# Performance work log

Hardware: AMD Instinct MI355X
Metric: run time of the kernel (lower is better)

## Reference

```python
import jax, jax.numpy as jnp
import numpy as np

T, D, H, E, V = 256, 512, 256, 256, 8192  # steps, max_ast_depth, hidden=units, emb dim, vocab


def setup_inputs() -> dict:
    key = jax.random.key(0)
    ks = jax.random.split(key, 12)
    s = 1.0 / np.sqrt(H)
    u = lambda k, shp: jax.random.uniform(k, shp, jnp.float32, -s, s)
    return {
        "nodes": jax.random.randint(ks[0], (T, D), 0, V),
        "edges": jax.random.randint(ks[1], (T, D), 0, 2).astype(bool),
        "initial_state": jax.random.normal(ks[2], (1, D, H), jnp.float32),
        "emb": jax.random.normal(ks[3], (V, E), jnp.float32) * 0.02,
        "c_Wih": u(ks[4], (3 * H, E)), "c_Whh": u(ks[5], (3 * H, H)),
        "c_bih": u(ks[6], (3 * H,)), "c_bhh": u(ks[7], (3 * H,)),
        "s_Wih": u(ks[8], (3 * H, E)), "s_Whh": u(ks[9], (3 * H, H)),
        "s_bih": u(ks[10], (3 * H,)), "s_bhh": u(ks[11], (3 * H,)),
    }


def _gru_cell(x, h, Wih, Whh, bih, bhh):
    # torch GRU cell math: gates ordered (r, z, n)
    gi = x @ Wih.T + bih           # [D, 3H]
    gh = h @ Whh.T + bhh           # [D, 3H]
    ir, iz, in_ = jnp.split(gi, 3, axis=-1)
    hr, hz, hn = jnp.split(gh, 3, axis=-1)
    r = jax.nn.sigmoid(ir + hr)
    z = jax.nn.sigmoid(iz + hz)
    n = jnp.tanh(in_ + r * hn)
    return (1.0 - z) * n + z * h   # [D, H]


def reference(nodes, edges, initial_state, emb,
              c_Wih, c_Whh, c_bih, c_bhh,
              s_Wih, s_Whh, s_bih, s_bhh):
    # Single-layer dual GRU: per step, run both GRUs on the same state and
    # route per node via the boolean edge mask (child vs sibling).
    def step(h, te):
        node_t, edge_t = te            # [D] int, [D] bool
        x = emb[node_t]                # [D, E] embedding gather
        hc = _gru_cell(x, h, c_Wih, c_Whh, c_bih, c_bhh)
        hs = _gru_cell(x, h, s_Wih, s_Whh, s_bih, s_bhh)
        h_new = jnp.where(edge_t[:, None], hc, hs)  # [D, H]
        return h_new, h_new            # output == new state for 1-layer GRU (seq_len 1)

    h_final, outs = jax.lax.scan(step, initial_state[0], (nodes, edges))
    # match torch shapes: outputs [T, D, 1, H], state [num_layers, D, H]
    return outs[:, :, None, :], h_final[None]
```

## Files before the change

kernel.cpp:

```cpp
#include <hip/hip_runtime.h>
#include <stdint.h>


#define TT   256
#define DDIM 512
#define LSTR 264

typedef float    float4v __attribute__((ext_vector_type(4)));
typedef short    short8  __attribute__((ext_vector_type(8)));
typedef uint32_t uint4v  __attribute__((ext_vector_type(4)));

__device__ __forceinline__ unsigned short f2bf(float f){
  uint32_t u = __float_as_uint(f);
  u += 0x7fffu + ((u >> 16) & 1u);
  return (unsigned short)(u >> 16);
}
__device__ __forceinline__ float bf2f(unsigned short h){
  return __uint_as_float(((uint32_t)h) << 16);
}

__global__ __launch_bounds__(256, 1)
void treernn_main(const int* __restrict__ nodes,
                  const unsigned char* __restrict__ edges,
                  const unsigned char* __restrict__ hinit,
                  const unsigned char* __restrict__ emb,
                  const unsigned char* __restrict__ cWih, const unsigned char* __restrict__ cWhh,
                  const unsigned char* __restrict__ cbih, const unsigned char* __restrict__ cbhh,
                  const unsigned char* __restrict__ sWih, const unsigned char* __restrict__ sWhh,
                  const unsigned char* __restrict__ sbih, const unsigned char* __restrict__ sbhh,
                  unsigned char* __restrict__ out,
                  unsigned char* __restrict__ ws)
{
  __shared__ __align__(16) unsigned short xs[2][32 * LSTR];
  __shared__ __align__(16) unsigned short hstg[32 * LSTR];
  __shared__ float hnewstg[32 * 17];
  __shared__ int det[8];

  const int tid   = threadIdx.x;
  const int lane  = tid & 63;
  const int wv    = tid >> 6;
  const int gru   = wv >> 1;
  const int mtile = wv & 1;
  const int quad  = lane >> 4;
  const int l16   = lane & 15;

  const int g     = blockIdx.x >> 4;
  const int slice = blockIdx.x & 15;
  const int col   = slice * 16 + l16;
  const int d0    = g * 32;
  const int rowb  = mtile * 16 + quad * 4;

  if (tid < 8) det[tid] = 0;
  __syncthreads();
  {
    const unsigned short* hu = (const unsigned short*)hinit;
    int ce = 0;
    for (int i = tid; i < 4096; i += 256){
      const int e = (hu[i] >> 7) & 0xFF;
      ce += (e >= 100 && e <= 130) ? 1 : 0;
    }
    atomicAdd(&det[0], ce);
    const uint32_t* ewp = (const uint32_t*)edges;
    int b01 = 0, w01 = 0, wf = 0, hb = 0;
    for (int i = tid; i < 512; i += 256){
      const uint32_t w = ewp[i];
      w01 += (w <= 1u) ? 1 : 0;
      wf  += (w == 0u || w == 0x3F800000u) ? 1 : 0;
      const uint32_t h0 = w & 0xFFFFu, h1 = w >> 16;
      hb  += ((h0 == 0u || h0 == 0x3F80u) ? 1 : 0) + ((h1 == 0u || h1 == 0x3F80u) ? 1 : 0);
      b01 += (((w      ) & 0xFFu) <= 1u ? 1 : 0) + (((w >> 8 ) & 0xFFu) <= 1u ? 1 : 0)
           + (((w >> 16) & 0xFFu) <= 1u ? 1 : 0) + (((w >> 24)        ) <= 1u ? 1 : 0);
    }
    atomicAdd(&det[1], b01); atomicAdd(&det[2], w01);
    atomicAdd(&det[3], wf);  atomicAdd(&det[4], hb);
  }
  __syncthreads();
  const int fdt = (det[0] >= 3480) ? 1 : 0;
  int efmt;
  if      (det[2] == 512)  efmt = 1;
  else if (det[1] == 2048) efmt = 0;
  else if (det[4] == 1024) efmt = 3;
  else if (det[3] == 512)  efmt = 2;
  else                     efmt = 0;

  uint32_t*       flg = (uint32_t*)ws;
  unsigned short* xb  = (unsigned short*)(ws + 8192);

  const unsigned char* Wihp = gru ? sWih : cWih;
  const unsigned char* Whhp = gru ? sWhh : cWhh;
  const unsigned char* bihp = gru ? sbih : cbih;
  const unsigned char* bhhp = gru ? sbhh : cbhh;

  float bI[3], bH[3];
  #pragma unroll
  for (int ga = 0; ga < 3; ++ga){
    if (fdt){
      bI[ga] = bf2f(((const unsigned short*)bihp)[ga * 256 + col]);
      bH[ga] = bf2f(((const unsigned short*)bhhp)[ga * 256 + col]);
    } else {
      bI[ga] = ((const float*)bihp)[ga * 256 + col];
      bH[ga] = ((const float*)bhhp)[ga * 256 + col];
    }
  }

  short8 wI[3][8], wH[3][8];
  for (int ga = 0; ga < 3; ++ga){
    const int rw = ga * 256 + col;
    for (int kc = 0; kc < 8; ++kc){
      const int ke = kc * 32 + quad * 8;
      if (fdt){
        wI[ga][kc] = *(const short8*)((const unsigned short*)Wihp + (size_t)rw * 256 + ke);
        wH[ga][kc] = *(const short8*)((const unsigned short*)Whhp + (size_t)rw * 256 + ke);
      } else {
        const float* pI = (const float*)Wihp + (size_t)rw * 256 + ke;
        const float* pH = (const float*)Whhp + (size_t)rw * 256 + ke;
        short8 va, vb;
        #pragma unroll
        for (int j = 0; j < 8; ++j){ va[j] = (short)f2bf(pI[j]); vb[j] = (short)f2bf(pH[j]); }
        wI[ga][kc] = va; wH[ga][kc] = vb;
      }
    }
  }

  {
    const int r = tid >> 3, c8 = (tid & 7) * 32;
    const int node = nodes[d0 + r];
    unsigned short* xdst = &xs[0][r * LSTR + c8];
    unsigned short* hdst = &hstg[r * LSTR + c8];
    if (fdt){
      const uint4v* sx = (const uint4v*)((const unsigned short*)emb   + (size_t)node * 256 + c8);
      const uint4v* sh = (const uint4v*)((const unsigned short*)hinit + (size_t)(d0 + r) * 256 + c8);
      #pragma unroll
      for (int j = 0; j < 4; ++j){ ((uint4v*)xdst)[j] = sx[j]; ((uint4v*)hdst)[j] = sh[j]; }
    } else {
      const float* sx = (const float*)emb   + (size_t)node * 256 + c8;
      const float* sh = (const float*)hinit + (size_t)(d0 + r) * 256 + c8;
      #pragma unroll
      for (int q = 0; q < 4; ++q){
        short8 vx, vh;
        #pragma unroll
        for (int j = 0; j < 8; ++j){ vx[j] = (short)f2bf(sx[q*8+j]); vh[j] = (short)f2bf(sh[q*8+j]); }
        *(short8*)&xdst[q * 8] = vx;
        *(short8*)&hdst[q * 8] = vh;
      }
    }
  }

  int ef[4];
  {
    const int base = d0 + rowb;
    if (efmt == 0){      for (int r = 0; r < 4; ++r) ef[r] = edges[base + r] != 0; }
    else if (efmt == 1){ for (int r = 0; r < 4; ++r) ef[r] = ((const int*)edges)[base + r] != 0; }
    else if (efmt == 3){ for (int r = 0; r < 4; ++r) ef[r] = ((const unsigned short*)edges)[base + r] != 0; }
    else {               for (int r = 0; r < 4; ++r) ef[r] = ((const float*)edges)[base + r] != 0.0f; }
  }
  __syncthreads();

  uint64_t gv[8];
  const int grow = tid >> 3;
  const int gchk = tid & 7;

  for (int t = 0; t < TT; ++t){
    if (slice == 0 && t >= 2){
      if (fdt){
        uint64_t* od = (uint64_t*)((unsigned short*)out + (size_t)(t - 2) * 131072
                                   + (size_t)(d0 + grow) * 256) + gchk;
        #pragma unroll
        for (int k = 0; k < 8; ++k) od[k * 8] = gv[k];
      } else {
        float* ob = (float*)out + (size_t)(t - 2) * 131072 + (size_t)(d0 + grow) * 256 + gchk * 4;
        #pragma unroll
        for (int k = 0; k < 8; ++k){
          float4v f;
          #pragma unroll
          for (int j = 0; j < 4; ++j) f[j] = bf2f((unsigned short)(gv[k] >> (16 * j)));
          *(float4v*)(ob + k * 32) = f;
        }
      }
    }

    float4v aI[3], aH[3];
    #pragma unroll
    for (int ga = 0; ga < 3; ++ga) aI[ga] = (float4v){bI[ga], bI[ga], bI[ga], bI[ga]};
    {
      const unsigned short* xc = xs[t & 1];
      #pragma unroll
      for (int kc = 0; kc < 8; ++kc){
        short8 a = *(const short8*)&xc[(mtile * 16 + l16) * LSTR + kc * 32 + quad * 8];
        #pragma unroll
        for (int ga = 0; ga < 3; ++ga)
          aI[ga] = __builtin_amdgcn_mfma_f32_16x16x32_bf16(a, wI[ga][kc], aI[ga], 0, 0, 0);
      }
    }

    float hold[4];
    if (t == 0){
      #pragma unroll
      for (int r = 0; r < 4; ++r){
        const size_t idx = (size_t)(d0 + rowb + r) * 256 + col;
        hold[r] = fdt ? bf2f(((const unsigned short*)hinit)[idx]) : ((const float*)hinit)[idx];
      }
    } else {
      #pragma unroll
      for (int r = 0; r < 4; ++r) hold[r] = hnewstg[(rowb + r) * 17 + l16];
    }

    if (t > 0){
      const uint32_t target = (uint32_t)t;
      const uint32_t* fp = flg + g * 64 + lane;
      uint32_t fv = __hip_atomic_load(fp, __ATOMIC_RELAXED, __HIP_MEMORY_SCOPE_AGENT);
      int guard = 0;
      while (__ballot(fv < target) != 0ull){
        __builtin_amdgcn_s_sleep(1);
        fv = __hip_atomic_load(fp, __ATOMIC_RELAXED, __HIP_MEMORY_SCOPE_AGENT);
        if (++guard > (1 << 17)) break;
      }
      __atomic_signal_fence(__ATOMIC_SEQ_CST);
      const uint64_t* src = (const uint64_t*)(xb + (size_t)(t & 1) * 131072
                                                 + (size_t)(d0 + grow) * 256) + gchk;
      #pragma unroll
      for (int k = 0; k < 8; ++k)
        gv[k] = __hip_atomic_load(src + k * 8, __ATOMIC_RELAXED, __HIP_MEMORY_SCOPE_AGENT);
      unsigned short* dst = &hstg[grow * LSTR + gchk * 4];
      #pragma unroll
      for (int k = 0; k < 8; ++k) *(uint64_t*)&dst[k * 32] = gv[k];
    }
    __syncthreads();

    #pragma unroll
    for (int ga = 0; ga < 3; ++ga) aH[ga] = (float4v){bH[ga], bH[ga], bH[ga], bH[ga]};
    #pragma unroll
    for (int kc = 0; kc < 8; ++kc){
      short8 a = *(const short8*)&hstg[(mtile * 16 + l16) * LSTR + kc * 32 + quad * 8];
      #pragma unroll
      for (int ga = 0; ga < 3; ++ga)
        aH[ga] = __builtin_amdgcn_mfma_f32_16x16x32_bf16(a, wH[ga][kc], aH[ga], 0, 0, 0);
    }

    float hnv[4]; int mine[4];
    #pragma unroll
    for (int r = 0; r < 4; ++r){
      const float pr = aI[0][r] + aH[0][r];
      const float pz = aI[1][r] + aH[1][r];
      const float R  = 1.0f / (1.0f + exp2f(-1.4426950408889634f * pr));
      const float Z  = 1.0f / (1.0f + exp2f(-1.4426950408889634f * pz));
      float ag = aI[2][r] + R * aH[2][r];
      ag = fminf(30.0f, fmaxf(-30.0f, ag));
      const float ex = exp2f(-2.8853900817779268f * ag);
      const float N  = (1.0f - ex) / (1.0f + ex);
      hnv[r]  = N + Z * (hold[r] - N);
      mine[r] = ((ef[r] != 0) == (gru == 0)) ? 1 : 0;
    }

    #pragma unroll
    for (int r = 0; r < 4; ++r){
      if (mine[r]) hnewstg[(rowb + r) * 17 + l16] = hnv[r];
      const uint32_t bb = (uint32_t)f2bf(hnv[r]);
      const uint32_t ob = (uint32_t)__shfl_xor((int)bb, 1, 64);
      if (mine[r] && !(lane & 1)){
        unsigned short* p = xb + (size_t)((t + 1) & 1) * 131072
                               + (size_t)(d0 + rowb + r) * 256 + col;
        __hip_atomic_store((uint32_t*)p, bb | (ob << 16),
                           __ATOMIC_RELAXED, __HIP_MEMORY_SCOPE_AGENT);
      }
    }

    __atomic_signal_fence(__ATOMIC_SEQ_CST);
    __builtin_amdgcn_s_waitcnt(0x0F70);
    __atomic_signal_fence(__ATOMIC_SEQ_CST);
    if (lane == 0)
      __hip_atomic_store(flg + g * 64 + slice * 4 + wv, (uint32_t)(t + 1),
                         __ATOMIC_RELAXED, __HIP_MEMORY_SCOPE_AGENT);

    if (t < TT - 1){
      const int r = tid >> 3, c8 = (tid & 7) * 32;
      const int node = nodes[(t + 1) * DDIM + d0 + r];
      unsigned short* dst = &xs[(t + 1) & 1][r * LSTR + c8];
      if (fdt){
        const uint4v* s = (const uint4v*)((const unsigned short*)emb + (size_t)node * 256 + c8);
        uint4v rv[4];
        #pragma unroll
        for (int j = 0; j < 4; ++j) rv[j] = s[j];
        #pragma unroll
        for (int j = 0; j < 4; ++j) ((uint4v*)dst)[j] = rv[j];
      } else {
        const float* s = (const float*)emb + (size_t)node * 256 + c8;
        float4v rv[8];
        #pragma unroll
        for (int j = 0; j < 8; ++j) rv[j] = ((const float4v*)s)[j];
        #pragma unroll
        for (int q = 0; q < 4; ++q){
          short8 v;
          #pragma unroll
          for (int j = 0; j < 8; ++j){ const int e2 = q*8+j; v[j] = (short)f2bf(rv[e2>>2][e2&3]); }
          *(short8*)&dst[q * 8] = v;
        }
      }
      const int base = (t + 1) * DDIM + d0 + rowb;
      if (efmt == 0){      for (int r2 = 0; r2 < 4; ++r2) ef[r2] = edges[base + r2] != 0; }
      else if (efmt == 1){ for (int r2 = 0; r2 < 4; ++r2) ef[r2] = ((const int*)edges)[base + r2] != 0; }
      else if (efmt == 3){ for (int r2 = 0; r2 < 4; ++r2) ef[r2] = ((const unsigned short*)edges)[base + r2] != 0; }
      else {               for (int r2 = 0; r2 < 4; ++r2) ef[r2] = ((const float*)edges)[base + r2] != 0.0f; }
    }

    __syncthreads();
  }

  if (slice == 0){
    if (fdt){
      uint64_t* od = (uint64_t*)((unsigned short*)out + (size_t)254 * 131072
                                 + (size_t)(d0 + grow) * 256) + gchk;
      #pragma unroll
      for (int k = 0; k < 8; ++k) od[k * 8] = gv[k];
    } else {
      float* ob = (float*)out + (size_t)254 * 131072 + (size_t)(d0 + grow) * 256 + gchk * 4;
      #pragma unroll
      for (int k = 0; k < 8; ++k){
        float4v f;
        #pragma unroll
        for (int j = 0; j < 4; ++j) f[j] = bf2f((unsigned short)(gv[k] >> (16 * j)));
        *(float4v*)(ob + k * 32) = f;
      }
    }

    const uint32_t* fp = flg + g * 64 + lane;
    uint32_t fv = __hip_atomic_load(fp, __ATOMIC_RELAXED, __HIP_MEMORY_SCOPE_AGENT);
    int guard = 0;
    while (__ballot(fv < 256u) != 0ull){
      __builtin_amdgcn_s_sleep(1);
      fv = __hip_atomic_load(fp, __ATOMIC_RELAXED, __HIP_MEMORY_SCOPE_AGENT);
      if (++guard > (1 << 17)) break;
    }
    __atomic_signal_fence(__ATOMIC_SEQ_CST);
    const uint64_t* src = (const uint64_t*)(xb +  (size_t)(d0 + grow) * 256) + gchk;
    uint64_t ev[8];
    #pragma unroll
    for (int k = 0; k < 8; ++k)
      ev[k] = __hip_atomic_load(src + k * 8, __ATOMIC_RELAXED, __HIP_MEMORY_SCOPE_AGENT);
    if (fdt){
      unsigned short* o16 = (unsigned short*)out;
      uint64_t* o1 = (uint64_t*)(o16 + (size_t)255 * 131072 + (size_t)(d0 + grow) * 256) + gchk;
      uint64_t* o2 = (uint64_t*)(o16 + (size_t)256 * 131072 + (size_t)(d0 + grow) * 256) + gchk;
      #pragma unroll
      for (int k = 0; k < 8; ++k){ o1[k * 8] = ev[k]; o2[k * 8] = ev[k]; }
    } else {
      float* o1 = (float*)out + (size_t)255 * 131072 + (size_t)(d0 + grow) * 256 + gchk * 4;
      float* o2 = (float*)out + (size_t)256 * 131072 + (size_t)(d0 + grow) * 256 + gchk * 4;
      #pragma unroll
      for (int k = 0; k < 8; ++k){
        float4v f;
        #pragma unroll
        for (int j = 0; j < 4; ++j) f[j] = bf2f((unsigned short)(ev[k] >> (16 * j)));
        *(float4v*)(o1 + k * 32) = f;
        *(float4v*)(o2 + k * 32) = f;
      }
    }
  }
}

extern "C" void kernel_launch(void* const* d_in, const int* in_sizes, int n_in,
                              void* d_out, int out_size, void* d_ws, size_t ws_size,
                              hipStream_t stream)
{
  const int*           nodes = (const int*)d_in[0];
  const unsigned char* edges = (const unsigned char*)d_in[1];
  const unsigned char* hinit = (const unsigned char*)d_in[2];
  const unsigned char* emb   = (const unsigned char*)d_in[3];
  const unsigned char* cWih  = (const unsigned char*)d_in[4];
  const unsigned char* cWhh  = (const unsigned char*)d_in[5];
  const unsigned char* cbih  = (const unsigned char*)d_in[6];
  const unsigned char* cbhh  = (const unsigned char*)d_in[7];
  const unsigned char* sWih  = (const unsigned char*)d_in[8];
  const unsigned char* sWhh  = (const unsigned char*)d_in[9];
  const unsigned char* sbih  = (const unsigned char*)d_in[10];
  const unsigned char* sbhh  = (const unsigned char*)d_in[11];
  (void)in_sizes; (void)n_in; (void)out_size; (void)ws_size;

  hipMemsetAsync(d_ws, 0, 8192, stream);

  treernn_main<<<dim3(256), dim3(256), 0, stream>>>(
      nodes, edges, hinit, emb, cWih, cWhh, cbih, cbhh, sWih, sWhh, sbih, sbhh,
      (unsigned char*)d_out, (unsigned char*)d_ws);
}
```

Before: 1.337 ms.

## Repartition GRU work into 16-row groups with 8 column slices per group

Each block now handles 16 rows and 32 output columns (8 slices per row group) instead of 32 rows and 16 columns. Every block writes its own output columns straight from registers rather than having slice 0 re-read the exchanged hidden state for the whole group. The previous hidden state is kept in shared memory, which drops the global read of hinit at t=0 inside the loop. The intent is to shrink per-block staging and the critical path of the per-step cross-block exchange, and to spread output stores across all blocks. In exchange the flag layout changes and output writes become narrower scattered 32-bit stores.

```diff
diff --git a/kernel.cpp b/kernel.cpp
--- a/kernel.cpp
+++ b/kernel.cpp
@@ -18,6 +18,7 @@
 __device__ __forceinline__ float bf2f(unsigned short h){
   return __uint_as_float(((uint32_t)h) << 16);
 }
+__device__ __forceinline__ float4v splat4(float v){ return (float4v){v, v, v, v}; }
 
 __global__ __launch_bounds__(256, 1)
 void treernn_main(const int* __restrict__ nodes,
@@ -31,24 +32,25 @@
                   unsigned char* __restrict__ out,
                   unsigned char* __restrict__ ws)
 {
-  __shared__ __align__(16) unsigned short xs[2][32 * LSTR];
-  __shared__ __align__(16) unsigned short hstg[32 * LSTR];
-  __shared__ float hnewstg[32 * 17];
+  __shared__ __align__(16) unsigned short xs[2][16 * LSTR];
+  __shared__ __align__(16) unsigned short hstg[16 * LSTR];
+  __shared__ float hold[16 * 33];
   __shared__ int det[8];
 
-  const int tid   = threadIdx.x;
-  const int lane  = tid & 63;
-  const int wv    = tid >> 6;
-  const int gru   = wv >> 1;
-  const int mtile = wv & 1;
-  const int quad  = lane >> 4;
-  const int l16   = lane & 15;
-
-  const int g     = blockIdx.x >> 4;
-  const int slice = blockIdx.x & 15;
-  const int col   = slice * 16 + l16;
-  const int d0    = g * 32;
-  const int rowb  = mtile * 16 + quad * 4;
+  const int tid  = threadIdx.x;
+  const int lane = tid & 63;
+  const int wv   = tid >> 6;
+  const int gru  = wv >> 1;
+  const int ch   = wv & 1;
+  const int quad = lane >> 4;
+  const int l16  = lane & 15;
+  const int bid  = blockIdx.x;
+
+  const int G    = bid >> 3;
+  const int cs   = bid & 7;
+  const int d0   = G * 16;
+  const int colw = ch * 16 + l16;
+  const int col  = cs * 32 + colw;
 
   if (tid < 8) det[tid] = 0;
   __syncthreads();
@@ -84,7 +86,7 @@
   else                     efmt = 0;
 
   uint32_t*       flg = (uint32_t*)ws;
-  unsigned short* xb  = (unsigned short*)(ws + 8192);
+  unsigned short* xbp = (unsigned short*)(ws + 16384);
 
   const unsigned char* Wihp = gru ? sWih : cWih;
   const unsigned char* Whhp = gru ? sWhh : cWhh;
@@ -123,32 +125,41 @@
   }
 
   {
-    const int r = tid >> 3, c8 = (tid & 7) * 32;
-    const int node = nodes[d0 + r];
-    unsigned short* xdst = &xs[0][r * LSTR + c8];
-    unsigned short* hdst = &hstg[r * LSTR + c8];
+    const int row = tid >> 4, cb = (tid & 15) * 16;
+    const int nd = nodes[d0 + row];
+    unsigned short* xdst = &xs[0][row * LSTR + cb];
+    unsigned short* hdst = &hstg[row * LSTR + cb];
     if (fdt){
-      const uint4v* sx = (const uint4v*)((const unsigned short*)emb   + (size_t)node * 256 + c8);
-      const uint4v* sh = (const uint4v*)((const unsigned short*)hinit + (size_t)(d0 + r) * 256 + c8);
-      #pragma unroll
-      for (int j = 0; j < 4; ++j){ ((uint4v*)xdst)[j] = sx[j]; ((uint4v*)hdst)[j] = sh[j]; }
+      const unsigned short* sx = (const unsigned short*)emb   + (size_t)nd * 256 + cb;
+      const unsigned short* sh = (const unsigned short*)hinit + (size_t)(d0 + row) * 256 + cb;
+      *(uint4v*)xdst       = *(const uint4v*)sx;
+      *(uint4v*)(xdst + 8) = *(const uint4v*)(sx + 8);
+      *(uint4v*)hdst       = *(const uint4v*)sh;
+      *(uint4v*)(hdst + 8) = *(const uint4v*)(sh + 8);
     } else {
-      const float* sx = (const float*)emb   + (size_t)node * 256 + c8;
-      const float* sh = (const float*)hinit + (size_t)(d0 + r) * 256 + c8;
-      #pragma unroll
-      for (int q = 0; q < 4; ++q){
-        short8 vx, vh;
-        #pragma unroll
-        for (int j = 0; j < 8; ++j){ vx[j] = (short)f2bf(sx[q*8+j]); vh[j] = (short)f2bf(sh[q*8+j]); }
-        *(short8*)&xdst[q * 8] = vx;
-        *(short8*)&hdst[q * 8] = vh;
-      }
-    }
-  }
-
+      const float* sx = (const float*)emb   + (size_t)nd * 256 + cb;
+      const float* sh = (const float*)hinit + (size_t)(d0 + row) * 256 + cb;
+      short8 v0, v1, w0, w1;
+      #pragma unroll
+      for (int j = 0; j < 8; ++j){
+        v0[j] = (short)f2bf(sx[j]); v1[j] = (short)f2bf(sx[8 + j]);
+        w0[j] = (short)f2bf(sh[j]); w1[j] = (short)f2bf(sh[8 + j]);
+      }
+      *(short8*)xdst = v0; *(short8*)(xdst + 8) = v1;
+      *(short8*)hdst = w0; *(short8*)(hdst + 8) = w1;
+    }
+    if (gru == 0){
+      #pragma unroll
+      for (int r = 0; r < 4; ++r){
+        const size_t si = (size_t)(d0 + quad * 4 + r) * 256 + col;
+        hold[(quad * 4 + r) * 33 + colw] =
+            fdt ? bf2f(((const unsigned short*)hinit)[si]) : ((const float*)hinit)[si];
+      }
+    }
+  }
   int ef[4];
   {
-    const int base = d0 + rowb;
+    const int base = d0 + quad * 4;
     if (efmt == 0){      for (int r = 0; r < 4; ++r) ef[r] = edges[base + r] != 0; }
     else if (efmt == 1){ for (int r = 0; r < 4; ++r) ef[r] = ((const int*)edges)[base + r] != 0; }
     else if (efmt == 3){ for (int r = 0; r < 4; ++r) ef[r] = ((const unsigned short*)edges)[base + r] != 0; }
@@ -156,58 +167,54 @@
   }
   __syncthreads();
 
-  uint64_t gv[8];
-  const int grow = tid >> 3;
-  const int gchk = tid & 7;
+  const int grow = tid >> 4;
+  const int gsub = tid & 15;
+  uint32_t* flgG = flg + G * 32;
+
+  uint32_t sPk[4] = {0, 0, 0, 0};
+  float    sCd[4] = {0, 0, 0, 0};
+  int      sMn[4] = {0, 0, 0, 0};
 
   for (int t = 0; t < TT; ++t){
-    if (slice == 0 && t >= 2){
-      if (fdt){
-        uint64_t* od = (uint64_t*)((unsigned short*)out + (size_t)(t - 2) * 131072
-                                   + (size_t)(d0 + grow) * 256) + gchk;
-        #pragma unroll
-        for (int k = 0; k < 8; ++k) od[k * 8] = gv[k];
-      } else {
-        float* ob = (float*)out + (size_t)(t - 2) * 131072 + (size_t)(d0 + grow) * 256 + gchk * 4;
-        #pragma unroll
-        for (int k = 0; k < 8; ++k){
-          float4v f;
-          #pragma unroll
-          for (int j = 0; j < 4; ++j) f[j] = bf2f((unsigned short)(gv[k] >> (16 * j)));
-          *(float4v*)(ob + k * 32) = f;
+    if (t > 0){
+      #pragma unroll
+      for (int r = 0; r < 4; ++r){
+        const int row = quad * 4 + r;
+        if (fdt){
+          if (sMn[r] && !(lane & 1)){
+            unsigned short* o16 = (unsigned short*)out;
+            *(uint32_t*)(o16 + (size_t)(t - 1) * 131072 + (size_t)(d0 + row) * 256 + col) = sPk[r];
+          }
+        } else {
+          if (sMn[r]){
+            float* o32 = (float*)out;
+            o32[(size_t)(t - 1) * 131072 + (size_t)(d0 + row) * 256 + col] = sCd[r];
+          }
         }
       }
     }
 
-    float4v aI[3], aH[3];
-    #pragma unroll
-    for (int ga = 0; ga < 3; ++ga) aI[ga] = (float4v){bI[ga], bI[ga], bI[ga], bI[ga]};
+    float4v aI[3];
+    #pragma unroll
+    for (int ga = 0; ga < 3; ++ga) aI[ga] = splat4(bI[ga]);
     {
       const unsigned short* xc = xs[t & 1];
       #pragma unroll
       for (int kc = 0; kc < 8; ++kc){
-        short8 a = *(const short8*)&xc[(mtile * 16 + l16) * LSTR + kc * 32 + quad * 8];
+        short8 a = *(const short8*)&xc[l16 * LSTR + kc * 32 + quad * 8];
         #pragma unroll
         for (int ga = 0; ga < 3; ++ga)
           aI[ga] = __builtin_amdgcn_mfma_f32_16x16x32_bf16(a, wI[ga][kc], aI[ga], 0, 0, 0);
       }
     }
 
-    float hold[4];
-    if (t == 0){
-      #pragma unroll
-      for (int r = 0; r < 4; ++r){
-        const size_t idx = (size_t)(d0 + rowb + r) * 256 + col;
-        hold[r] = fdt ? bf2f(((const unsigned short*)hinit)[idx]) : ((const float*)hinit)[idx];
-      }
-    } else {
-      #pragma unroll
-      for (int r = 0; r < 4; ++r) hold[r] = hnewstg[(rowb + r) * 17 + l16];
-    }
+    float hold4[4];
+    #pragma unroll
+    for (int r = 0; r < 4; ++r) hold4[r] = hold[(quad * 4 + r) * 33 + colw];
 
     if (t > 0){
       const uint32_t target = (uint32_t)t;
-      const uint32_t* fp = flg + g * 64 + lane;
+      const uint32_t* fp = flgG + (lane & 31);
       uint32_t fv = __hip_atomic_load(fp, __ATOMIC_RELAXED, __HIP_MEMORY_SCOPE_AGENT);
       int guard = 0;
       while (__ballot(fv < target) != 0ull){
@@ -216,28 +223,32 @@
         if (++guard > (1 << 17)) break;
       }
       __atomic_signal_fence(__ATOMIC_SEQ_CST);
-      const uint64_t* src = (const uint64_t*)(xb + (size_t)(t & 1) * 131072
-                                                 + (size_t)(d0 + grow) * 256) + gchk;
-      #pragma unroll
-      for (int k = 0; k < 8; ++k)
-        gv[k] = __hip_atomic_load(src + k * 8, __ATOMIC_RELAXED, __HIP_MEMORY_SCOPE_AGENT);
-      unsigned short* dst = &hstg[grow * LSTR + gchk * 4];
-      #pragma unroll
-      for (int k = 0; k < 8; ++k) *(uint64_t*)&dst[k * 32] = gv[k];
+      const uint64_t* src = (const uint64_t*)(xbp + ((size_t)(t & 1) * 512 + d0 + grow) * 256
+                                                  + gsub * 16);
+      uint64_t a0 = __hip_atomic_load(src + 0, __ATOMIC_RELAXED, __HIP_MEMORY_SCOPE_AGENT);
+      uint64_t a1 = __hip_atomic_load(src + 1, __ATOMIC_RELAXED, __HIP_MEMORY_SCOPE_AGENT);
+      uint64_t a2 = __hip_atomic_load(src + 2, __ATOMIC_RELAXED, __HIP_MEMORY_SCOPE_AGENT);
+      uint64_t a3 = __hip_atomic_load(src + 3, __ATOMIC_RELAXED, __HIP_MEMORY_SCOPE_AGENT);
+      unsigned short* dst = &hstg[grow * LSTR + gsub * 16];
+      *(uint64_t*)(dst + 0)  = a0;
+      *(uint64_t*)(dst + 4)  = a1;
+      *(uint64_t*)(dst + 8)  = a2;
+      *(uint64_t*)(dst + 12) = a3;
     }
     __syncthreads();
 
-    #pragma unroll
-    for (int ga = 0; ga < 3; ++ga) aH[ga] = (float4v){bH[ga], bH[ga], bH[ga], bH[ga]};
+    float4v aH[3];
+    #pragma unroll
+    for (int ga = 0; ga < 3; ++ga) aH[ga] = splat4(bH[ga]);
     #pragma unroll
     for (int kc = 0; kc < 8; ++kc){
-      short8 a = *(const short8*)&hstg[(mtile * 16 + l16) * LSTR + kc * 32 + quad * 8];
+      short8 a = *(const short8*)&hstg[l16 * LSTR + kc * 32 + quad * 8];
       #pragma unroll
       for (int ga = 0; ga < 3; ++ga)
         aH[ga] = __builtin_amdgcn_mfma_f32_16x16x32_bf16(a, wH[ga][kc], aH[ga], 0, 0, 0);
     }
 
-    float hnv[4]; int mine[4];
+    float cand[4]; int mine[4];
     #pragma unroll
     for (int r = 0; r < 4; ++r){
       const float pr = aI[0][r] + aH[0][r];
@@ -248,111 +259,76 @@
       ag = fminf(30.0f, fmaxf(-30.0f, ag));
       const float ex = exp2f(-2.8853900817779268f * ag);
       const float N  = (1.0f - ex) / (1.0f + ex);
-      hnv[r]  = N + Z * (hold[r] - N);
+      cand[r] = N + Z * (hold4[r] - N);
       mine[r] = ((ef[r] != 0) == (gru == 0)) ? 1 : 0;
     }
 
+    const int buf = (t + 1) & 1;
     #pragma unroll
     for (int r = 0; r < 4; ++r){
-      if (mine[r]) hnewstg[(rowb + r) * 17 + l16] = hnv[r];
-      const uint32_t bb = (uint32_t)f2bf(hnv[r]);
+      const int row = quad * 4 + r;
+      if (mine[r]) hold[row * 33 + colw] = cand[r];
+      const uint32_t bb = (uint32_t)f2bf(cand[r]);
       const uint32_t ob = (uint32_t)__shfl_xor((int)bb, 1, 64);
-      if (mine[r] && !(lane & 1)){
-        unsigned short* p = xb + (size_t)((t + 1) & 1) * 131072
-                               + (size_t)(d0 + rowb + r) * 256 + col;
-        __hip_atomic_store((uint32_t*)p, bb | (ob << 16),
+      const uint32_t pk = bb | (ob << 16);
+      sPk[r] = pk; sCd[r] = cand[r]; sMn[r] = mine[r];
+      if (t < TT - 1 && mine[r] && !(lane & 1)){
+        uint32_t* xp = (uint32_t*)&xbp[((size_t)buf * 512 + d0 + row) * 256 + col];
+        __hip_atomic_store(xp, pk, __ATOMIC_RELAXED, __HIP_MEMORY_SCOPE_AGENT);
+      }
+    }
+
+    if (t < TT - 1){
+      __atomic_signal_fence(__ATOMIC_SEQ_CST);
+      __builtin_amdgcn_s_waitcnt(0x0F70);
+      __atomic_signal_fence(__ATOMIC_SEQ_CST);
+      if (lane == 0)
+        __hip_atomic_store(flgG + cs * 4 + wv, (uint32_t)(t + 1),
                            __ATOMIC_RELAXED, __HIP_MEMORY_SCOPE_AGENT);
-      }
-    }
-
-    __atomic_signal_fence(__ATOMIC_SEQ_CST);
-    __builtin_amdgcn_s_waitcnt(0x0F70);
-    __atomic_signal_fence(__ATOMIC_SEQ_CST);
-    if (lane == 0)
-      __hip_atomic_store(flg + g * 64 + slice * 4 + wv, (uint32_t)(t + 1),
-                         __ATOMIC_RELAXED, __HIP_MEMORY_SCOPE_AGENT);
-
-    if (t < TT - 1){
-      const int r = tid >> 3, c8 = (tid & 7) * 32;
-      const int node = nodes[(t + 1) * DDIM + d0 + r];
-      unsigned short* dst = &xs[(t + 1) & 1][r * LSTR + c8];
-      if (fdt){
-        const uint4v* s = (const uint4v*)((const unsigned short*)emb + (size_t)node * 256 + c8);
-        uint4v rv[4];
-        #pragma unroll
-        for (int j = 0; j < 4; ++j) rv[j] = s[j];
-        #pragma unroll
-        for (int j = 0; j < 4; ++j) ((uint4v*)dst)[j] = rv[j];
-      } else {
-        const float* s = (const float*)emb + (size_t)node * 256 + c8;
-        float4v rv[8];
-        #pragma unroll
-        for (int j = 0; j < 8; ++j) rv[j] = ((const float4v*)s)[j];
-        #pragma unroll
-        for (int q = 0; q < 4; ++q){
-          short8 v;
+
+      {
+        const int row = tid >> 4, cb = (tid & 15) * 16;
+        const int nd = nodes[(t + 1) * DDIM + d0 + row];
+        unsigned short* dst = &xs[buf][row * LSTR + cb];
+        if (fdt){
+          const unsigned short* s = (const unsigned short*)emb + (size_t)nd * 256 + cb;
+          uint4v r0 = *(const uint4v*)s;
+          uint4v r1 = *(const uint4v*)(s + 8);
+          *(uint4v*)dst       = r0;
+          *(uint4v*)(dst + 8) = r1;
+        } else {
+          const float* s = (const float*)emb + (size_t)nd * 256 + cb;
+          short8 v0, v1;
           #pragma unroll
-          for (int j = 0; j < 8; ++j){ const int e2 = q*8+j; v[j] = (short)f2bf(rv[e2>>2][e2&3]); }
-          *(short8*)&dst[q * 8] = v;
+          for (int j = 0; j < 8; ++j){ v0[j] = (short)f2bf(s[j]); v1[j] = (short)f2bf(s[8 + j]); }
+          *(short8*)dst       = v0;
+          *(short8*)(dst + 8) = v1;
         }
-      }
-      const int base = (t + 1) * DDIM + d0 + rowb;
-      if (efmt == 0){      for (int r2 = 0; r2 < 4; ++r2) ef[r2] = edges[base + r2] != 0; }
-      else if (efmt == 1){ for (int r2 = 0; r2 < 4; ++r2) ef[r2] = ((const int*)edges)[base + r2] != 0; }
-      else if (efmt == 3){ for (int r2 = 0; r2 < 4; ++r2) ef[r2] = ((const unsigned short*)edges)[base + r2] != 0; }
-      else {               for (int r2 = 0; r2 < 4; ++r2) ef[r2] = ((const float*)edges)[base + r2] != 0.0f; }
+        const int eb = (t + 1) * DDIM + d0 + quad * 4;
+        if (efmt == 0){      for (int r2 = 0; r2 < 4; ++r2) ef[r2] = edges[eb + r2] != 0; }
+        else if (efmt == 1){ for (int r2 = 0; r2 < 4; ++r2) ef[r2] = ((const int*)edges)[eb + r2] != 0; }
+        else if (efmt == 3){ for (int r2 = 0; r2 < 4; ++r2) ef[r2] = ((const unsigned short*)edges)[eb + r2] != 0; }
+        else {               for (int r2 = 0; r2 < 4; ++r2) ef[r2] = ((const float*)edges)[eb + r2] != 0.0f; }
+      }
     }
 
     __syncthreads();
   }
 
-  if (slice == 0){
+  #pragma unroll
+  for (int r = 0; r < 4; ++r){
+    const int row = quad * 4 + r;
     if (fdt){
-      uint64_t* od = (uint64_t*)((unsigned short*)out + (size_t)254 * 131072
-                                 + (size_t)(d0 + grow) * 256) + gchk;
-      #pragma unroll
-      for (int k = 0; k < 8; ++k) od[k * 8] = gv[k];
+      if (sMn[r] && !(lane & 1)){
+        unsigned short* o16 = (unsigned short*)out;
+        *(uint32_t*)(o16 + (size_t)255 * 131072 + (size_t)(d0 + row) * 256 + col) = sPk[r];
+        *(uint32_t*)(o16 + (size_t)256 * 131072 + (size_t)(d0 + row) * 256 + col) = sPk[r];
+      }
     } else {
-      float* ob = (float*)out + (size_t)254 * 131072 + (size_t)(d0 + grow) * 256 + gchk * 4;
-      #pragma unroll
-      for (int k = 0; k < 8; ++k){
-        float4v f;
-        #pragma unroll
-        for (int j = 0; j < 4; ++j) f[j] = bf2f((unsigned short)(gv[k] >> (16 * j)));
-        *(float4v*)(ob + k * 32) = f;
-      }
-    }
-
-    const uint32_t* fp = flg + g * 64 + lane;
-    uint32_t fv = __hip_atomic_load(fp, __ATOMIC_RELAXED, __HIP_MEMORY_SCOPE_AGENT);
-    int guard = 0;
-    while (__ballot(fv < 256u) != 0ull){
-      __builtin_amdgcn_s_sleep(1);
-      fv = __hip_atomic_load(fp, __ATOMIC_RELAXED, __HIP_MEMORY_SCOPE_AGENT);
-      if (++guard > (1 << 17)) break;
-    }
-    __atomic_signal_fence(__ATOMIC_SEQ_CST);
-    const uint64_t* src = (const uint64_t*)(xb +  (size_t)(d0 + grow) * 256) + gchk;
-    uint64_t ev[8];
-    #pragma unroll
-    for (int k = 0; k < 8; ++k)
-      ev[k] = __hip_atomic_load(src + k * 8, __ATOMIC_RELAXED, __HIP_MEMORY_SCOPE_AGENT);
-    if (fdt){
-      unsigned short* o16 = (unsigned short*)out;
-      uint64_t* o1 = (uint64_t*)(o16 + (size_t)255 * 131072 + (size_t)(d0 + grow) * 256) + gchk;
-      uint64_t* o2 = (uint64_t*)(o16 + (size_t)256 * 131072 + (size_t)(d0 + grow) * 256) + gchk;
-      #pragma unroll
-      for (int k = 0; k < 8; ++k){ o1[k * 8] = ev[k]; o2[k * 8] = ev[k]; }
-    } else {
-      float* o1 = (float*)out + (size_t)255 * 131072 + (size_t)(d0 + grow) * 256 + gchk * 4;
-      float* o2 = (float*)out + (size_t)256 * 131072 + (size_t)(d0 + grow) * 256 + gchk * 4;
-      #pragma unroll
-      for (int k = 0; k < 8; ++k){
-        float4v f;
-        #pragma unroll
-        for (int j = 0; j < 4; ++j) f[j] = bf2f((unsigned short)(ev[k] >> (16 * j)));
-        *(float4v*)(o1 + k * 32) = f;
-        *(float4v*)(o2 + k * 32) = f;
+      if (sMn[r]){
+        float* o32 = (float*)out;
+        o32[(size_t)255 * 131072 + (size_t)(d0 + row) * 256 + col] = sCd[r];
+        o32[(size_t)256 * 131072 + (size_t)(d0 + row) * 256 + col] = sCd[r];
       }
     }
   }
```

New measurement: 1.258 ms. 1.06x faster.
